# Performance work log

Measured on AMD Instinct MI355X. Metric: run time of the kernel, lower is better.

The kernel has to match this reference:

```python
import jax, jax.numpy as jnp
import numpy as np

H = 16          # num_heads
D = 64          # head_dim = dim // num_heads
ROPE_THETA = 10000.0
NEG = -1e9


def _rope_angles(n, d):
    # matches get_1d_rotary_pos_embed(head_dim, N): freqs_cis = polar(1, t outer (theta^-(2i/d)))
    inv_freq = 1.0 / (ROPE_THETA ** (jnp.arange(0, d, 2, dtype=jnp.float32) / d))  # [d/2]
    ang = jnp.arange(n, dtype=jnp.float32)[:, None] * inv_freq[None, :]            # [n, d/2]
    return jnp.cos(ang), jnp.sin(ang)


def _apply_rope(x, cos, sin):
    # x: [B,H,N,D]; complex rotation on adjacent pairs (use_real=False semantics)
    x0 = x[..., 0::2]
    x1 = x[..., 1::2]
    # broadcast cos/sin [N, D/2] over batch and heads
    r0 = x0 * cos - x1 * sin
    r1 = x0 * sin + x1 * cos
    return jnp.stack([r0, r1], axis=-1).reshape(x.shape)


def setup_inputs() -> dict:
    key = jax.random.key(0)
    ks = jax.random.split(key, 5)
    B, N, C = 4, 2048, 1024
    s_in = 1.0 / np.sqrt(C)
    return {
        "x": jax.random.normal(ks[0], (B, N, C), dtype=jnp.float32),
        "Wqkv_w": jax.random.normal(ks[1], (3 * C, C), dtype=jnp.float32) * s_in,
        "Wqkv_b": jax.random.normal(ks[2], (3 * C,), dtype=jnp.float32) * 0.01,
        "out_w": jax.random.normal(ks[3], (C, C), dtype=jnp.float32) * s_in,
        "out_b": jax.random.normal(ks[4], (C,), dtype=jnp.float32) * 0.01,
    }


def reference(x, Wqkv_w, Wqkv_b, out_w, out_b):
    B, N, C = x.shape
    scale = D ** -0.5
    # fused QKV projection: [B,N,3C] -> [3,B,H,N,D]
    qkv = (jnp.einsum('bnc,oc->bno', x, Wqkv_w) + Wqkv_b)
    qkv = qkv.reshape(B, N, 3, H, D).transpose(2, 0, 3, 1, 4)
    q, k, v = qkv[0], qkv[1], qkv[2]
    # qk_norm=False -> Identity
    cos, sin = _rope_angles(N, D)
    q = _apply_rope(q, cos, sin)
    k = _apply_rope(k, cos, sin)
    attn = jnp.einsum('bhqd,bhkd->bhqk', q * scale, k)      # [B,H,N,N]
    causal = jnp.triu(jnp.ones((N, N), dtype=bool), k=1)
    attn = jnp.where(causal[None, None], NEG, attn)
    attn = jax.nn.softmax(attn, axis=-1)
    o = jnp.einsum('bhqk,bhkd->bhqd', attn, v)              # [B,H,N,D]
    o = o.transpose(0, 2, 1, 3).reshape(B, N, C)
    return jnp.einsum('bnc,oc->bno', o, out_w) + out_b
```

## Files before the change

### kernel.cpp

```cpp
#include <hip/hip_runtime.h>
#include <hip/hip_bf16.h>

#define DEVI __device__ __forceinline__

typedef __attribute__((ext_vector_type(8))) short short8v;
typedef __attribute__((ext_vector_type(4))) float f32x4;
typedef __attribute__((ext_vector_type(2))) unsigned u32x2;

DEVI short f2bf(float f) {
  __hip_bfloat16 h = __float2bfloat16(f);
  return __builtin_bit_cast(short, h);
}
DEVI float bf2f(short s) {
  unsigned u = ((unsigned)(unsigned short)s) << 16;
  return __builtin_bit_cast(float, u);
}
DEVI unsigned packbf(float a, float b) {
  return (unsigned)(unsigned short)f2bf(a) | ((unsigned)(unsigned short)f2bf(b) << 16);
}
DEVI void gload16(const void* g, void* l) {
  __builtin_amdgcn_global_load_lds((const __attribute__((address_space(1))) void*)g,
                                   (__attribute__((address_space(3))) void*)l, 16, 0, 0);
}
#define MFMA16(a, b, c) __builtin_amdgcn_mfma_f32_16x16x32_bf16((a), (b), (c), 0, 0, 0)


__global__ void cvt_all(const float* __restrict__ x, const float* __restrict__ wq,
                        const float* __restrict__ wo, short* __restrict__ xb,
                        short* __restrict__ wqb, short* __restrict__ wob) {
  int i = blockIdx.x * blockDim.x + threadIdx.x;
  const float* in;
  short* out;
  if (i < 2097152) { in = x; out = xb; }
  else if (i < 2097152 + 786432) { in = wq; out = wqb; i -= 2097152; }
  else { in = wo; out = wob; i -= 2097152 + 786432; }
  float4 v = ((const float4*)in)[i];
  short4 o;
  o.x = f2bf(v.x); o.y = f2bf(v.y); o.z = f2bf(v.z); o.w = f2bf(v.w);
  ((short4*)out)[i] = o;
}

__global__ void rope_table(float2* __restrict__ tbl) {
  int i = blockIdx.x * blockDim.x + threadIdx.x;
  int n = i >> 5, f = i & 31;
  float inv = powf(10000.0f, -(float)f * (1.0f / 32.0f));
  float ang = (float)n * inv;
  tbl[i] = make_float2(cosf(ang), sinf(ang));
}

__global__ void rope_k(short* __restrict__ kk, const float2* __restrict__ tbl) {
  int i = blockIdx.x * blockDim.x + threadIdx.x;
  int row = i >> 3, c8 = i & 7;
  int n = row & 2047;
  short* ad = kk + (size_t)row * 64 + c8 * 8;
  short8v vv = *(short8v*)ad;
  short8v ov;
#pragma unroll
  for (int j = 0; j < 4; ++j) {
    float2 cs = tbl[n * 32 + c8 * 4 + j];
    float x0 = bf2f(vv[2 * j]), x1 = bf2f(vv[2 * j + 1]);
    ov[2 * j]     = f2bf(x0 * cs.x - x1 * cs.y);
    ov[2 * j + 1] = f2bf(x0 * cs.y + x1 * cs.x);
  }
  *(short8v*)ad = ov;
}

template <int EPI>
__global__ __launch_bounds__(256)
void gemm_bt(const short* __restrict__ A, const short* __restrict__ Bw,
             const float* __restrict__ bias,
             short* __restrict__ q, short* __restrict__ k, short* __restrict__ v,
             float* __restrict__ fout, int Mdim, int Ndim, int Kdim) {
  __shared__ __attribute__((aligned(16))) short As[3][128 * 32];
  __shared__ __attribute__((aligned(16))) short Bs[3][128 * 32];
  const int t = threadIdx.x;
  const int lane = t & 63, w = t >> 6;
  const int wr = w >> 1, wc = w & 1;
  const int g = lane >> 4, r16 = lane & 15;
  const int m0 = blockIdx.y * 128, n0 = blockIdx.x * 128;

  int goffs[2], loffs[2];
#pragma unroll
  for (int p = 0; p < 2; ++p) {
    int c = p * 256 + t;
    int row = c >> 2, u = c & 3;
    goffs[p] = row * Kdim + ((u ^ ((row >> 1) & 3)) * 8);
    loffs[p] = c * 16;
  }
  const short* Abase = A + (size_t)m0 * Kdim;
  const short* Bbase = Bw + (size_t)n0 * Kdim;

  auto STAGE = [&](int s, int k0) {
#pragma unroll
    for (int p = 0; p < 2; ++p) {
      gload16(Abase + k0 + goffs[p], (char*)&As[s][0] + loffs[p]);
      gload16(Bbase + k0 + goffs[p], (char*)&Bs[s][0] + loffs[p]);
    }
  };

  f32x4 acc[4][4];
#pragma unroll
  for (int i = 0; i < 4; ++i)
#pragma unroll
    for (int j = 0; j < 4; ++j) acc[i][j] = (f32x4){0.f, 0.f, 0.f, 0.f};

  const int nsteps = Kdim >> 5;
  STAGE(0, 0);
  STAGE(1, 32);
  asm volatile("s_waitcnt vmcnt(4)" ::: "memory");
  __builtin_amdgcn_s_barrier();
  asm volatile("" ::: "memory");

  int cur = 0, pre = 2;
  const int rsw = (r16 >> 1) & 3;
  for (int st = 0; st < nsteps; ++st) {
    if (st + 2 < nsteps) STAGE(pre, (st + 2) << 5);
    short8v af[4], bf[4];
#pragma unroll
    for (int mi = 0; mi < 4; ++mi)
      af[mi] = *(const short8v*)&As[cur][(wr * 64 + mi * 16 + r16) * 32 +
                                         ((g ^ rsw) * 8)];
#pragma unroll
    for (int ni = 0; ni < 4; ++ni)
      bf[ni] = *(const short8v*)&Bs[cur][(wc * 64 + ni * 16 + r16) * 32 +
                                         ((g ^ rsw) * 8)];
#pragma unroll
    for (int mi = 0; mi < 4; ++mi)
#pragma unroll
      for (int ni = 0; ni < 4; ++ni)
        acc[mi][ni] = MFMA16(af[mi], bf[ni], acc[mi][ni]);
    if (st + 2 < nsteps) asm volatile("s_waitcnt vmcnt(4)" ::: "memory");
    else                 asm volatile("s_waitcnt vmcnt(0)" ::: "memory");
    __builtin_amdgcn_s_barrier();
    asm volatile("" ::: "memory");
    cur = (cur == 2) ? 0 : cur + 1;
    pre = (pre == 2) ? 0 : pre + 1;
  }

  if (EPI == 0) {
#pragma unroll
    for (int ni = 0; ni < 4; ++ni) {
      int col = n0 + wc * 64 + ni * 16 + r16;
      float bv = bias[col];
      int s = col >> 10, rr = col & 1023, h = rr >> 6, d = rr & 63;
      short* dst = (s == 0) ? q : (s == 1 ? k : v);
      const bool vt = (s == 2);
#pragma unroll
      for (int mi = 0; mi < 4; ++mi) {
        int mrow = m0 + wr * 64 + mi * 16 + g * 4;
#pragma unroll
        for (int r = 0; r < 4; ++r) {
          int m = mrow + r;
          int b = m >> 11, n = m & 2047;
          size_t idx = vt ? ((((size_t)(b * 16 + h)) * 64 + d) * 2048 + n)
                          : ((((size_t)(b * 16 + h)) * 2048 + n) * 64 + d);
          dst[idx] = f2bf(acc[mi][ni][r] + bv);
        }
      }
    }
  } else {
#pragma unroll
    for (int ni = 0; ni < 4; ++ni) {
      int col = n0 + wc * 64 + ni * 16 + r16;
      float bv = bias[col];
#pragma unroll
      for (int mi = 0; mi < 4; ++mi) {
        int mrow = m0 + wr * 64 + mi * 16 + g * 4;
#pragma unroll
        for (int r = 0; r < 4; ++r)
          fout[(size_t)(mrow + r) * Ndim + col] = acc[mi][ni][r] + bv;
      }
    }
  }
}

__global__ __launch_bounds__(256)
void fattn(const short* __restrict__ q, const short* __restrict__ k,
           const short* __restrict__ vT, const float2* __restrict__ tbl,
           short* __restrict__ o) {
  const int bx = blockIdx.x;
  const int qt = 15 - (bx >> 6);
  const int bh = bx & 63;
  const int b = bh >> 4, h = bh & 15;
  const int t = threadIdx.x, lane = t & 63, w = t >> 6;
  const int g = lane >> 4, r16 = lane & 15;

  __shared__ __attribute__((aligned(16))) short Ks[2][64 * 64];
  __shared__ __attribute__((aligned(16))) short Vt[2][64 * 64];
  __shared__ __attribute__((aligned(16))) short Ps[4][2][16 * 72];

  const short* qb = q + (size_t)bh * 2048 * 64;
  const short* kb = k + (size_t)bh * 2048 * 64;
  const short* vb = vT + (size_t)bh * 2048 * 64;

  int koffs[2], voffs[2], loffs[2];
#pragma unroll
  for (int p = 0; p < 2; ++p) {
    int c = p * 256 + t;
    int row = c >> 3, u = c & 7;
    int x8 = (u ^ (row & 7)) * 8;
    koffs[p] = row * 64 + x8;
    voffs[p] = row * 2048 + x8;
    loffs[p] = c * 16;
  }
  auto STAGE = [&](int s, int kt) {
#pragma unroll
    for (int p = 0; p < 2; ++p) {
      gload16(kb + (size_t)kt * 4096 + koffs[p], (char*)&Ks[s][0] + loffs[p]);
      gload16(vb + kt * 64 + voffs[p], (char*)&Vt[s][0] + loffs[p]);
    }
  };

  const int q0 = qt * 128 + w * 32;

  const float sc = 0.125f * 1.44269504088896f;
  short8v aq[2][2];
#pragma unroll
  for (int qi = 0; qi < 2; ++qi) {
    const int n = q0 + qi * 16 + r16;
#pragma unroll
    for (int dk = 0; dk < 2; ++dk) {
      short8v raw = *(const short8v*)(qb + (size_t)n * 64 + dk * 32 + g * 8);
      short8v rq;
#pragma unroll
      for (int j = 0; j < 4; ++j) {
        float2 cs = tbl[n * 32 + dk * 16 + g * 4 + j];
        float x0 = bf2f(raw[2 * j]), x1 = bf2f(raw[2 * j + 1]);
        rq[2 * j]     = f2bf((x0 * cs.x - x1 * cs.y) * sc);
        rq[2 * j + 1] = f2bf((x0 * cs.y + x1 * cs.x) * sc);
      }
      aq[qi][dk] = rq;
    }
  }

  const short one_bf = 0x3F80;
  const short8v ones = {one_bf, one_bf, one_bf, one_bf, one_bf, one_bf, one_bf, one_bf};
  const float M = 24.0f;

  f32x4 oacc[2][4], lacc[2];
#pragma unroll
  for (int qi = 0; qi < 2; ++qi) {
#pragma unroll
    for (int dc = 0; dc < 4; ++dc) oacc[qi][dc] = (f32x4){0.f, 0.f, 0.f, 0.f};
    lacc[qi] = (f32x4){0.f, 0.f, 0.f, 0.f};
  }

  const int ktmax = 2 * qt + 1;

  STAGE(0, 0);
  __syncthreads();

  for (int kt = 0; kt <= ktmax; ++kt) {
    const int cur = kt & 1;
    if (kt < ktmax) STAGE(cur ^ 1, kt + 1);

    const bool act0 = (kt * 64 <= q0 + 15);
    const bool act1 = (kt * 64 <= q0 + 31);

    f32x4 s[2][4];
#pragma unroll
    for (int qi = 0; qi < 2; ++qi)
#pragma unroll
      for (int kc = 0; kc < 4; ++kc) s[qi][kc] = (f32x4){0.f, 0.f, 0.f, 0.f};

    if (act1) {
#pragma unroll
      for (int kc = 0; kc < 4; ++kc) {
        int key = kc * 16 + r16;
        const char* rb = (const char*)&Ks[cur][0] + key * 128;
        short8v kf0 = *(const short8v*)(rb + (((g) ^ (key & 7)) << 4));
        short8v kf1 = *(const short8v*)(rb + (((4 + g) ^ (key & 7)) << 4));
        if (act0) {
          s[0][kc] = MFMA16(kf0, aq[0][0], s[0][kc]);
          s[0][kc] = MFMA16(kf1, aq[0][1], s[0][kc]);
        }
        s[1][kc] = MFMA16(kf0, aq[1][0], s[1][kc]);
        s[1][kc] = MFMA16(kf1, aq[1][1], s[1][kc]);
      }

#pragma unroll
      for (int qi = 0; qi < 2; ++qi) {
        if (qi == 0 && !act0) continue;
        const int qrow = q0 + qi * 16 + r16;
        const bool needmask = (kt * 64 + 63 > q0 + qi * 16);
        if (needmask) {
#pragma unroll
          for (int kc = 0; kc < 4; ++kc)
#pragma unroll
            for (int r = 0; r < 4; ++r)
              if (kt * 64 + kc * 16 + g * 4 + r > qrow) s[qi][kc][r] = -1e30f;
        }
        unsigned pk[4][2];
#pragma unroll
        for (int kc = 0; kc < 4; ++kc) {
          float p0 = __builtin_amdgcn_exp2f(s[qi][kc][0] - M);
          float p1 = __builtin_amdgcn_exp2f(s[qi][kc][1] - M);
          float p2 = __builtin_amdgcn_exp2f(s[qi][kc][2] - M);
          float p3 = __builtin_amdgcn_exp2f(s[qi][kc][3] - M);
          pk[kc][0] = packbf(p0, p1);
          pk[kc][1] = packbf(p2, p3);
        }
#pragma unroll
        for (int kc = 0; kc < 4; ++kc)
          *(u32x2*)((char*)&Ps[w][qi][0] + r16 * 144 + kc * 32 + g * 8) =
              (u32x2){pk[kc][0], pk[kc][1]};
      }

      asm volatile("" ::: "memory");

      short8v pa[2][2];
#pragma unroll
      for (int qi = 0; qi < 2; ++qi) {
        if (qi == 0 && !act0) continue;
#pragma unroll
        for (int kk = 0; kk < 2; ++kk)
          pa[qi][kk] =
              *(const short8v*)((char*)&Ps[w][qi][0] + r16 * 144 + kk * 64 + g * 16);
      }
      if (act0) {
        lacc[0] = MFMA16(pa[0][0], ones, lacc[0]);
        lacc[0] = MFMA16(pa[0][1], ones, lacc[0]);
      }
      lacc[1] = MFMA16(pa[1][0], ones, lacc[1]);
      lacc[1] = MFMA16(pa[1][1], ones, lacc[1]);
#pragma unroll
      for (int dc = 0; dc < 4; ++dc) {
        int d = dc * 16 + r16;
        const char* vr = (const char*)&Vt[cur][0] + d * 128;
#pragma unroll
        for (int kk = 0; kk < 2; ++kk) {
          short8v bv = *(const short8v*)(vr + (((kk * 4 + g) ^ (d & 7)) << 4));
          if (act0) oacc[0][dc] = MFMA16(pa[0][kk], bv, oacc[0][dc]);
          oacc[1][dc] = MFMA16(pa[1][kk], bv, oacc[1][dc]);
        }
      }
    }
    __syncthreads();
  }

#pragma unroll
  for (int qi = 0; qi < 2; ++qi) {
#pragma unroll
    for (int r = 0; r < 4; ++r) {
      float ilr = 1.f / lacc[qi][r];
      int qg = q0 + qi * 16 + g * 4 + r;
      short* orow = o + ((size_t)(b * 2048 + qg)) * 1024 + h * 64;
#pragma unroll
      for (int dc = 0; dc < 4; ++dc)
        orow[dc * 16 + r16] = f2bf(oacc[qi][dc][r] * ilr);
    }
  }
}

extern "C" void kernel_launch(void* const* d_in, const int* in_sizes, int n_in,
                              void* d_out, int out_size, void* d_ws, size_t ws_size,
                              hipStream_t stream) {
  const float* x    = (const float*)d_in[0];
  const float* Wqkv = (const float*)d_in[1];
  const float* bqkv = (const float*)d_in[2];
  const float* Wout = (const float*)d_in[3];
  const float* bout = (const float*)d_in[4];

  char* p = (char*)d_ws;
  short* xb = (short*)p;    p += (size_t)8192 * 1024 * 2;
  short* wqkvb = (short*)p; p += (size_t)3072 * 1024 * 2;
  short* woutb = (short*)p; p += (size_t)1024 * 1024 * 2;
  short* qbf = (short*)p;   p += (size_t)64 * 2048 * 64 * 2;
  short* kbf = (short*)p;   p += (size_t)64 * 2048 * 64 * 2;
  short* vbf = (short*)p;   p += (size_t)64 * 2048 * 64 * 2;
  float2* tbl = (float2*)p; p += (size_t)2048 * 32 * 8;

  cvt_all<<<12288, 256, 0, stream>>>(x, Wqkv, Wout, xb, wqkvb, woutb);
  rope_table<<<256, 256, 0, stream>>>(tbl);

  gemm_bt<0><<<dim3(24, 64), 256, 0, stream>>>(xb, wqkvb, bqkv, qbf, kbf, vbf, nullptr,
                                               8192, 3072, 1024);
  rope_k<<<4096, 256, 0, stream>>>(kbf, tbl);
  fattn<<<dim3(1024), 256, 0, stream>>>(qbf, kbf, vbf, tbl, xb);
  gemm_bt<1><<<dim3(8, 64), 256, 0, stream>>>(xb, woutb, bout, nullptr, nullptr, nullptr,
                                              (float*)d_out, 8192, 1024, 1024);
}
```

Measured before the change: 206.2 us.

## Stage V-transpose epilogue through LDS and raise wave priority around MFMA blocks

The QKV GEMM epilogue for the V slice now goes through a shared-memory tile. The tile is transposed there, and threads write coalesced 16-byte chunks into the transposed V layout. Before, each thread did scattered 2-byte stores with a stride of 2048 elements. The attention kernel also wraps its QK and PV MFMA sections in s_setprio to favour matrix-issuing waves. The staging adds an extra LDS buffer and two barriers per half-tile in the V blocks.

```diff
diff --git a/kernel.cpp b/kernel.cpp
--- a/kernel.cpp
+++ b/kernel.cpp
@@ -138,23 +138,53 @@
   }
 
   if (EPI == 0) {
-#pragma unroll
-    for (int ni = 0; ni < 4; ++ni) {
-      int col = n0 + wc * 64 + ni * 16 + r16;
-      float bv = bias[col];
-      int s = col >> 10, rr = col & 1023, h = rr >> 6, d = rr & 63;
-      short* dst = (s == 0) ? q : (s == 1 ? k : v);
-      const bool vt = (s == 2);
-#pragma unroll
-      for (int mi = 0; mi < 4; ++mi) {
-        int mrow = m0 + wr * 64 + mi * 16 + g * 4;
-#pragma unroll
-        for (int r = 0; r < 4; ++r) {
-          int m = mrow + r;
-          int b = m >> 11, n = m & 2047;
-          size_t idx = vt ? ((((size_t)(b * 16 + h)) * 64 + d) * 2048 + n)
-                          : ((((size_t)(b * 16 + h)) * 2048 + n) * 64 + d);
-          dst[idx] = f2bf(acc[mi][ni][r] + bv);
+    if (n0 >= 2048) {
+      __shared__ __attribute__((aligned(16))) short Cs[64][136];
+      const int b = m0 >> 11;
+      const int nb = m0 & 2047;
+#pragma unroll
+      for (int hh = 0; hh < 2; ++hh) {
+        if (wc == hh) {
+#pragma unroll
+          for (int ni = 0; ni < 4; ++ni) {
+            float bv = bias[n0 + hh * 64 + ni * 16 + r16];
+#pragma unroll
+            for (int mi = 0; mi < 4; ++mi) {
+              u32x2 pk;
+              pk[0] = packbf(acc[mi][ni][0] + bv, acc[mi][ni][1] + bv);
+              pk[1] = packbf(acc[mi][ni][2] + bv, acc[mi][ni][3] + bv);
+              *(u32x2*)&Cs[ni * 16 + r16][wr * 64 + mi * 16 + g * 4] = pk;
+            }
+          }
+        }
+        __syncthreads();
+        const int hdr = ((n0 + hh * 64) & 1023) >> 6;
+        short* vdst = v + ((size_t)(b * 16 + hdr)) * 64 * 2048;
+#pragma unroll
+        for (int j = 0; j < 4; ++j) {
+          int chunk = j * 256 + t;
+          int d = chunk >> 4, c16 = chunk & 15;
+          short8v val = *(const short8v*)&Cs[d][c16 * 8];
+          *(short8v*)(vdst + (size_t)d * 2048 + nb + c16 * 8) = val;
+        }
+        __syncthreads();
+      }
+    } else {
+#pragma unroll
+      for (int ni = 0; ni < 4; ++ni) {
+        int col = n0 + wc * 64 + ni * 16 + r16;
+        float bv = bias[col];
+        int s = col >> 10, rr = col & 1023, h = rr >> 6, d = rr & 63;
+        short* dst = (s == 0) ? q : k;
+#pragma unroll
+        for (int mi = 0; mi < 4; ++mi) {
+          int mrow = m0 + wr * 64 + mi * 16 + g * 4;
+#pragma unroll
+          for (int r = 0; r < 4; ++r) {
+            int m = mrow + r;
+            int b = m >> 11, n = m & 2047;
+            dst[(((size_t)(b * 16 + h)) * 2048 + n) * 64 + d] = f2bf(acc[mi][ni][r] + bv);
+          }
         }
       }
     }
@@ -264,6 +294,7 @@
       for (int kc = 0; kc < 4; ++kc) s[qi][kc] = (f32x4){0.f, 0.f, 0.f, 0.f};
 
     if (act1) {
+      __builtin_amdgcn_s_setprio(1);
 #pragma unroll
       for (int kc = 0; kc < 4; ++kc) {
         int key = kc * 16 + r16;
@@ -277,6 +308,7 @@
         s[1][kc] = MFMA16(kf0, aq[1][0], s[1][kc]);
         s[1][kc] = MFMA16(kf1, aq[1][1], s[1][kc]);
       }
+      __builtin_amdgcn_s_setprio(0);
 
 #pragma unroll
       for (int qi = 0; qi < 2; ++qi) {
@@ -317,6 +349,7 @@
           pa[qi][kk] =
               *(const short8v*)((char*)&Ps[w][qi][0] + r16 * 144 + kk * 64 + g * 16);
       }
+      __builtin_amdgcn_s_setprio(1);
       if (act0) {
         lacc[0] = MFMA16(pa[0][0], ones, lacc[0]);
         lacc[0] = MFMA16(pa[0][1], ones, lacc[0]);
@@ -334,6 +367,7 @@
           oacc[1][dc] = MFMA16(pa[1][kk], bv, oacc[1][dc]);
         }
       }
+      __builtin_amdgcn_s_setprio(0);
     }
     __syncthreads();
   }
```

After: 194.2 us. 1.06x faster.
